# Optimization experiments

Measured on AMD Instinct MI355X. Metric: run time of the kernel, lower is better.

## Reference

```python
import jax, jax.numpy as jnp
import numpy as np


def setup_inputs() -> dict:
    key = jax.random.key(0)
    k1, k2, k3 = jax.random.split(key, 3)
    N, E, C, OUT = 100000, 1000000, 64, 64
    x = jax.random.normal(k1, (N, C), dtype=jnp.float32)
    edge_index = jax.random.randint(k2, (2, E), 0, N, dtype=jnp.int32)
    W = jax.random.normal(k3, (2 * C, OUT), dtype=jnp.float32) * (1.0 / np.sqrt(2 * C))
    b = jnp.zeros((OUT,), dtype=jnp.float32)
    return {"x": x, "edge_index": edge_index, "W": W, "b": b}


def reference(x, edge_index, W, b):
    # MRConv: x_j = scatter_max(x[src] - x[dst], dst); out = relu(cat([x, x_j]) @ W + b)
    N = x.shape[0]
    src, dst = edge_index[0], edge_index[1]
    diff = x[src] - x[dst]                                  # [E, C] gather + diff
    x_j = jax.ops.segment_max(diff, dst, num_segments=N)    # [N, C] scatter-max
    # nodes with no incoming edges get -inf from segment_max; tg fills them with 0
    x_j = jnp.where(jnp.isfinite(x_j), x_j, 0.0)
    h = jnp.concatenate([x, x_j], axis=1)                   # [N, 2C]
    return jax.nn.relu(h @ W + b)                           # [N, OUT]
```

## Files before the change

kernel.cpp:

```cpp
#include <hip/hip_runtime.h>
#include <math.h>

#define SENT 0x007FFFFFu
#define NEGINF_BITS 0xFF800000u
#define NA 256
#define SB_SHIFT 5
#define SB_MASK ((1u << SB_SHIFT) - 1u)
#define NB 32
#define PITCH 68
#define MAXSB 4096
#define CGRID 1024
#define PADROW 32u

typedef __attribute__((ext_vector_type(8))) short bf16x8;
typedef __attribute__((ext_vector_type(4))) float f32x4;

__device__ __forceinline__ unsigned int fmap(float f) {
    unsigned int u = __float_as_uint(f);
    return (u & 0x80000000u) ? ~u : (u | 0x80000000u);
}
__device__ __forceinline__ unsigned int fmap_bits(unsigned int u) {
    return (u & 0x80000000u) ? ~u : (u | 0x80000000u);
}
__device__ __forceinline__ float funmap(unsigned int u) {
    unsigned int bits = (u & 0x80000000u) ? (u ^ 0x80000000u) : ~u;
    return __uint_as_float(bits);
}
__device__ __forceinline__ unsigned short tobf(float f) {
    unsigned int u = __float_as_uint(f);
    u += 0x7FFFu + ((u >> 16) & 1u);
    return (unsigned short)(u >> 16);
}
__device__ __forceinline__ float frombf(unsigned short s) {
    return __uint_as_float((unsigned int)s << 16);
}

__global__ void __launch_bounds__(256) casthist_kernel(const float* __restrict__ x,
                                                       unsigned short* __restrict__ xb,
                                                       long long n,
                                                       const int* __restrict__ ei,
                                                       unsigned* __restrict__ counts2,
                                                       int E, int nsb, int chunk, int cgrid) {
    __shared__ unsigned h[MAXSB];
    if ((int)blockIdx.x < cgrid) {
        long long i = ((long long)blockIdx.x * 256 + threadIdx.x) * 8;
        long long stride = (long long)cgrid * 256 * 8;
        for (; i < n; i += stride) {
            float4 a = *(const float4*)(x + i);
            float4 c = *(const float4*)(x + i + 4);
            uint4 o;
            o.x = (unsigned)tobf(a.x) | ((unsigned)tobf(a.y) << 16);
            o.y = (unsigned)tobf(a.z) | ((unsigned)tobf(a.w) << 16);
            o.z = (unsigned)tobf(c.x) | ((unsigned)tobf(c.y) << 16);
            o.w = (unsigned)tobf(c.z) | ((unsigned)tobf(c.w) << 16);
            *(uint4*)(xb + i) = o;
        }
    } else {
        int hb = (int)blockIdx.x - cgrid;
        for (int t = threadIdx.x; t < nsb; t += 256) h[t] = 0u;
        __syncthreads();
        int beg = hb * chunk;
        int end = min(beg + chunk, E);
        for (int i = beg + threadIdx.x; i < end; i += 256)
            atomicAdd(&h[((unsigned)ei[E + i]) >> SB_SHIFT], 1u);
        __syncthreads();
        for (int t = threadIdx.x; t < nsb; t += 256)
            counts2[(size_t)t * NA + hb] = h[t];
    }
}

__global__ void __launch_bounds__(256) histA_kernel(const int* __restrict__ ei,
                                                    unsigned* __restrict__ counts2,
                                                    int E, int nsb, int chunk) {
    __shared__ unsigned h[MAXSB];
    for (int t = threadIdx.x; t < nsb; t += 256) h[t] = 0u;
    __syncthreads();
    int beg = blockIdx.x * chunk;
    int end = min(beg + chunk, E);
    for (int i = beg + threadIdx.x; i < end; i += 256)
        atomicAdd(&h[((unsigned)ei[E + i]) >> SB_SHIFT], 1u);
    __syncthreads();
    for (int t = threadIdx.x; t < nsb; t += 256)
        counts2[(size_t)t * NA + blockIdx.x] = h[t];
}

__global__ void __launch_bounds__(512) rowscan_kernel(unsigned* __restrict__ counts2,
                                                      unsigned* __restrict__ sbtot, int nsb) {
    int lane = threadIdx.x & 63;
    int sb = blockIdx.x * 8 + (threadIdx.x >> 6);
    if (sb >= nsb) return;
    unsigned* row = counts2 + (size_t)sb * NA;
    uint4 v = *(const uint4*)(row + 4 * lane);
    unsigned local = v.x + v.y + v.z + v.w;
    unsigned incl = local;
    #pragma unroll
    for (int d = 1; d < 64; d <<= 1) {
        unsigned t = __shfl_up(incl, d);
        if (lane >= d) incl += t;
    }
    unsigned e0 = incl - local;
    uint4 o;
    o.x = e0;
    o.y = e0 + v.x;
    o.z = o.y + v.y;
    o.w = o.z + v.z;
    *(uint4*)(row + 4 * lane) = o;
    if (lane == 63) sbtot[sb] = incl;
}

__global__ void __launch_bounds__(1024) sbscan_kernel(const unsigned* __restrict__ sbtot,
                                                      unsigned* __restrict__ sbbase, int nsb) {
    __shared__ unsigned s[1024];
    __shared__ unsigned carry_s;
    if (threadIdx.x == 0) carry_s = 0u;
    __syncthreads();
    for (int chunk = 0; chunk < nsb; chunk += 1024) {
        int i = chunk + threadIdx.x;
        unsigned v = (i < nsb) ? ((sbtot[i] + 15u) & ~15u) : 0u;
        s[threadIdx.x] = v;
        __syncthreads();
        for (int d = 1; d < 1024; d <<= 1) {
            unsigned t = (threadIdx.x >= d) ? s[threadIdx.x - d] : 0u;
            __syncthreads();
            s[threadIdx.x] += t;
            __syncthreads();
        }
        unsigned carry = carry_s;
        if (i < nsb) sbbase[i] = carry + s[threadIdx.x] - v;
        __syncthreads();
        if (threadIdx.x == 1023) carry_s = carry + s[1023];
        __syncthreads();
    }
    if (threadIdx.x == 0) sbbase[nsb] = carry_s;
}

__global__ void __launch_bounds__(256) placeB_kernel(const int* __restrict__ ei,
                                                     const unsigned* __restrict__ counts2,
                                                     const unsigned* __restrict__ sbbase,
                                                     unsigned* __restrict__ ssrc,
                                                     int E, int nsb, int chunk) {
    __shared__ unsigned fill[MAXSB];
    for (int t = threadIdx.x; t < nsb; t += 256)
        fill[t] = sbbase[t] + counts2[(size_t)t * NA + blockIdx.x];
    __syncthreads();
    int beg = blockIdx.x * chunk;
    int end = min(beg + chunk, E);
    for (int i = beg + threadIdx.x; i < end; i += 256) {
        unsigned src = (unsigned)ei[i];
        unsigned dst = (unsigned)ei[E + i];
        unsigned pos = atomicAdd(&fill[dst >> SB_SHIFT], 1u);
        ssrc[pos] = (src << 6) | (dst & SB_MASK);
    }
}

__global__ void __launch_bounds__(256) pad_kernel(const unsigned* __restrict__ sbbase,
                                                  const unsigned* __restrict__ sbtot,
                                                  unsigned* __restrict__ ssrc, int nsb) {
    int i = blockIdx.x * blockDim.x + threadIdx.x;
    if (i >= nsb) return;
    unsigned s = sbbase[i] + sbtot[i];
    unsigned e = sbbase[i + 1];
    for (unsigned j = s; j < e; ++j) ssrc[j] = PADROW;
}

__global__ void __launch_bounds__(256) reduceBf_kernel(const unsigned short* __restrict__ xb,
                                                       const unsigned* __restrict__ sbbase,
                                                       const unsigned* __restrict__ ssrc,
                                                       unsigned short* __restrict__ xj, int N) {
    __shared__ unsigned M[(NB + 1) * PITCH];
    int tid = threadIdx.x;
    int lane = tid & 63;
    int wid = tid >> 6;

    for (int i = tid; i < (NB + 1) * PITCH; i += 256) M[i] = SENT;

    int nodeBase = blockIdx.x * NB;
    int beg = (int)sbbase[blockIdx.x];
    int end = (int)sbbase[blockIdx.x + 1];
    __syncthreads();

    for (int i0 = beg + wid * 16; i0 < end; i0 += 64) {
        int si = __builtin_amdgcn_readfirstlane(i0);
        uint4 q0 = *(const uint4*)(ssrc + si);
        uint4 q1 = *(const uint4*)(ssrc + si + 4);
        uint4 q2 = *(const uint4*)(ssrc + si + 8);
        uint4 q3 = *(const uint4*)(ssrc + si + 12);
        unsigned pp[16] = {q0.x, q0.y, q0.z, q0.w, q1.x, q1.y, q1.z, q1.w,
                           q2.x, q2.y, q2.z, q2.w, q3.x, q3.y, q3.z, q3.w};
        unsigned short vv[16];
        #pragma unroll
        for (int k = 0; k < 16; ++k)
            vv[k] = xb[(pp[k] & 0xFFFFFFC0u) | (unsigned)lane];
        #pragma unroll
        for (int k = 0; k < 16; ++k) {
            unsigned u32 = ((unsigned)vv[k]) << 16;
            atomicMax(&M[(pp[k] & 63u) * PITCH + lane], fmap_bits(u32));
        }
    }
    __syncthreads();

    for (int row = wid; row < NB; row += 4) {
        int n = nodeBase + row;
        if (n < N) {
            unsigned um = M[row * PITCH + lane];
            unsigned short o = 0;
            if (um != SENT) {
                float mx = funmap(um);
                float xv = frombf(xb[(size_t)n * 64 + lane]);
                o = tobf(mx - xv);
            }
            xj[(size_t)n * 64 + lane] = o;
        }
    }
}

__global__ void __launch_bounds__(256) mlpBf_kernel(const unsigned short* __restrict__ xb,
                                                    const unsigned short* __restrict__ xj,
                                                    const float* __restrict__ W,
                                                    const float* __restrict__ b,
                                                    float* __restrict__ out, int N) {
    int lane = threadIdx.x & 63;
    int wid  = threadIdx.x >> 6;
    int r = lane & 15;
    int g = lane >> 4;

    bf16x8 Bf[4][4];
    #pragma unroll
    for (int nt = 0; nt < 4; ++nt)
        #pragma unroll
        for (int kt = 0; kt < 4; ++kt) {
            const float* wp = W + (size_t)(kt * 32 + g * 8) * 64 + nt * 16 + r;
            bf16x8 f;
            #pragma unroll
            for (int j = 0; j < 8; ++j) f[j] = (short)tobf(wp[(size_t)j * 64]);
            Bf[nt][kt] = f;
        }
    float bias[4];
    #pragma unroll
    for (int nt = 0; nt < 4; ++nt) bias[nt] = b[nt * 16 + r];

    int nTiles = (N + 15) >> 4;
    int totalWaves = gridDim.x * 4;
    for (int tile = blockIdx.x * 4 + wid; tile < nTiles; tile += totalWaves) {
        int nodeBase = tile << 4;
        int rowIdx = min(nodeBase + r, N - 1);
        const unsigned short* xp = xb + (size_t)rowIdx * 64;
        const unsigned short* jp = xj + (size_t)rowIdx * 64;

        bf16x8 Af[4];
        #pragma unroll
        for (int kt = 0; kt < 2; ++kt) {
            Af[kt]     = *(const bf16x8*)(xp + kt * 32 + g * 8);
            Af[2 + kt] = *(const bf16x8*)(jp + kt * 32 + g * 8);
        }

        f32x4 acc[4];
        #pragma unroll
        for (int nt = 0; nt < 4; ++nt) {
            f32x4 a = {bias[nt], bias[nt], bias[nt], bias[nt]};
            acc[nt] = a;
        }
        #pragma unroll
        for (int nt = 0; nt < 4; ++nt)
            #pragma unroll
            for (int kt = 0; kt < 4; ++kt)
                acc[nt] = __builtin_amdgcn_mfma_f32_16x16x32_bf16(Af[kt], Bf[nt][kt], acc[nt], 0, 0, 0);

        #pragma unroll
        for (int nt = 0; nt < 4; ++nt)
            #pragma unroll
            for (int reg = 0; reg < 4; ++reg) {
                int nrow = nodeBase + g * 4 + reg;
                if (nrow < N)
                    out[(size_t)nrow * 64 + nt * 16 + r] = fmaxf(acc[nt][reg], 0.0f);
            }
    }
}


__global__ void __launch_bounds__(256) reduceB_kernel(const float* __restrict__ x,
                                                      const unsigned* __restrict__ sbbase,
                                                      const unsigned* __restrict__ ssrc,
                                                      float* __restrict__ xj, int N) {
    __shared__ unsigned M[(NB + 1) * PITCH];
    int tid = threadIdx.x;
    int lane = tid & 63;
    int wid = tid >> 6;

    for (int i = tid; i < (NB + 1) * PITCH; i += 256) M[i] = SENT;

    int nodeBase = blockIdx.x * NB;
    int beg = (int)sbbase[blockIdx.x];
    int end = (int)sbbase[blockIdx.x + 1];
    __syncthreads();

    for (int i0 = beg + wid * 16; i0 < end; i0 += 64) {
        int si = __builtin_amdgcn_readfirstlane(i0);
        uint4 q0 = *(const uint4*)(ssrc + si);
        uint4 q1 = *(const uint4*)(ssrc + si + 4);
        uint4 q2 = *(const uint4*)(ssrc + si + 8);
        uint4 q3 = *(const uint4*)(ssrc + si + 12);
        unsigned pp[16] = {q0.x, q0.y, q0.z, q0.w, q1.x, q1.y, q1.z, q1.w,
                           q2.x, q2.y, q2.z, q2.w, q3.x, q3.y, q3.z, q3.w};
        float vv[16];
        #pragma unroll
        for (int k = 0; k < 16; ++k)
            vv[k] = x[(pp[k] & 0xFFFFFFC0u) | (unsigned)lane];
        #pragma unroll
        for (int k = 0; k < 16; ++k)
            atomicMax(&M[(pp[k] & 63u) * PITCH + lane], fmap(vv[k]));
    }
    __syncthreads();

    for (int row = wid; row < NB; row += 4) {
        int n = nodeBase + row;
        if (n < N) xj[(size_t)n * 64 + lane] = funmap(M[row * PITCH + lane]);
    }
}

template <bool MAPPED>
__global__ void __launch_bounds__(256) mlp_kernel(const float* __restrict__ x,
                                                  const unsigned int* xj,
                                                  const float* __restrict__ W,
                                                  const float* __restrict__ b,
                                                  float* out, int N) {
    int lane = threadIdx.x & 63;
    int wid  = threadIdx.x >> 6;
    int r = lane & 15;
    int g = lane >> 4;

    bf16x8 Bf[4][4];
    #pragma unroll
    for (int nt = 0; nt < 4; ++nt)
        #pragma unroll
        for (int kt = 0; kt < 4; ++kt) {
            const float* wp = W + (size_t)(kt * 32 + g * 8) * 64 + nt * 16 + r;
            bf16x8 f;
            #pragma unroll
            for (int j = 0; j < 8; ++j) f[j] = (short)tobf(wp[(size_t)j * 64]);
            Bf[nt][kt] = f;
        }
    float bias[4];
    #pragma unroll
    for (int nt = 0; nt < 4; ++nt) bias[nt] = b[nt * 16 + r];

    int nTiles = (N + 15) >> 4;
    int totalWaves = gridDim.x * 4;
    for (int tile = blockIdx.x * 4 + wid; tile < nTiles; tile += totalWaves) {
        int nodeBase = tile << 4;
        int rowIdx = min(nodeBase + r, N - 1);
        const float* xp = x + (size_t)rowIdx * 64;
        const unsigned int* jp = xj + (size_t)rowIdx * 64;

        bf16x8 Af[4];
        float xs[2][8];
        #pragma unroll
        for (int kt = 0; kt < 2; ++kt) {
            float4 flo = *(const float4*)(xp + kt * 32 + g * 8);
            float4 fhi = *(const float4*)(xp + kt * 32 + g * 8 + 4);
            xs[kt][0] = flo.x; xs[kt][1] = flo.y; xs[kt][2] = flo.z; xs[kt][3] = flo.w;
            xs[kt][4] = fhi.x; xs[kt][5] = fhi.y; xs[kt][6] = fhi.z; xs[kt][7] = fhi.w;
            bf16x8 f;
            #pragma unroll
            for (int j = 0; j < 8; ++j) f[j] = (short)tobf(xs[kt][j]);
            Af[kt] = f;
        }
        #pragma unroll
        for (int kt = 0; kt < 2; ++kt) {
            uint4 ulo = *(const uint4*)(jp + kt * 32 + g * 8);
            uint4 uhi = *(const uint4*)(jp + kt * 32 + g * 8 + 4);
            unsigned int uu[8] = {ulo.x, ulo.y, ulo.z, ulo.w, uhi.x, uhi.y, uhi.z, uhi.w};
            bf16x8 f;
            #pragma unroll
            for (int j = 0; j < 8; ++j) {
                bool empty;
                float v;
                if (MAPPED) { empty = (uu[j] == SENT); v = funmap(uu[j]); }
                else        { empty = (uu[j] == NEGINF_BITS); v = __uint_as_float(uu[j]); }
                f[j] = (short)tobf(empty ? 0.0f : (v - xs[kt][j]));
            }
            Af[2 + kt] = f;
        }

        f32x4 acc[4];
        #pragma unroll
        for (int nt = 0; nt < 4; ++nt) {
            f32x4 a = {bias[nt], bias[nt], bias[nt], bias[nt]};
            acc[nt] = a;
        }
        #pragma unroll
        for (int nt = 0; nt < 4; ++nt)
            #pragma unroll
            for (int kt = 0; kt < 4; ++kt)
                acc[nt] = __builtin_amdgcn_mfma_f32_16x16x32_bf16(Af[kt], Bf[nt][kt], acc[nt], 0, 0, 0);

        #pragma unroll
        for (int nt = 0; nt < 4; ++nt)
            #pragma unroll
            for (int reg = 0; reg < 4; ++reg) {
                int nrow = nodeBase + g * 4 + reg;
                if (nrow < N)
                    out[(size_t)nrow * 64 + nt * 16 + r] = fmaxf(acc[nt][reg], 0.0f);
            }
    }
}


__global__ void init_kernel(uint4* __restrict__ ws, int n4) {
    int i = blockIdx.x * blockDim.x + threadIdx.x;
    int stride = gridDim.x * blockDim.x;
    uint4 v = make_uint4(SENT, SENT, SENT, SENT);
    for (; i < n4; i += stride) ws[i] = v;
}

__global__ void scatter_kernel(const float* __restrict__ x,
                               const int* __restrict__ ei,
                               unsigned int* __restrict__ ws, int E) {
    long long gid = (long long)blockIdx.x * blockDim.x + threadIdx.x;
    int e = (int)(gid >> 6);
    int lane = (int)(gid & 63);
    if (e >= E) return;
    int src = ei[e];
    int dst = ei[E + e];
    unsigned int m = fmap(x[(size_t)src * 64 + lane]);
    unsigned int* p = ws + (size_t)dst * 64 + lane;
    if (m > *p) atomicMax(p, m);
}

extern "C" void kernel_launch(void* const* d_in, const int* in_sizes, int n_in,
                              void* d_out, int out_size, void* d_ws, size_t ws_size,
                              hipStream_t stream) {
    const float* x  = (const float*)d_in[0];
    const int*   ei = (const int*)d_in[1];
    const float* W  = (const float*)d_in[2];
    const float* b  = (const float*)d_in[3];
    float* out = (float*)d_out;

    int N = in_sizes[0] / 64;
    int E = in_sizes[1] / 2;

    int nsb = (N + NB - 1) >> SB_SHIFT;
    int chunk = (E + NA - 1) / NA;

    size_t counts2_b = (size_t)nsb * NA * 4;
    size_t sbtot_b   = (size_t)((nsb + 63) & ~63) * 4;
    size_t sbbase_b  = (size_t)(nsb + 1 + 63) / 64 * 64 * 4;
    size_t ssrc_b    = ((size_t)E + 16u * (size_t)nsb) * 4;
    size_t xb_b      = (size_t)N * 64 * 2;
    size_t xjb_b     = (size_t)N * 64 * 2;
    size_t xj32_b    = (size_t)N * 64 * 4;
    size_t needB     = counts2_b + sbtot_b + sbbase_b + ssrc_b;
    size_t needA     = needB + xb_b + xjb_b;

    int mgrid = (((N + 15) >> 4) + 3) / 4;

    if (ws_size >= needA && nsb <= MAXSB) {
        char* p = (char*)d_ws;
        unsigned* counts2 = (unsigned*)p; p += counts2_b;
        unsigned* sbtot   = (unsigned*)p; p += sbtot_b;
        unsigned* sbbase  = (unsigned*)p; p += sbbase_b;
        unsigned* ssrc    = (unsigned*)p; p += ssrc_b;
        unsigned short* xb  = (unsigned short*)p; p += xb_b;
        unsigned short* xjb = (unsigned short*)p;

        long long n = (long long)N * 64;
        casthist_kernel<<<CGRID + NA, 256, 0, stream>>>(x, xb, n, ei, counts2, E, nsb, chunk, CGRID);
        rowscan_kernel<<<(nsb + 7) / 8, 512, 0, stream>>>(counts2, sbtot, nsb);
        sbscan_kernel<<<1, 1024, 0, stream>>>(sbtot, sbbase, nsb);
        placeB_kernel<<<NA, 256, 0, stream>>>(ei, counts2, sbbase, ssrc, E, nsb, chunk);
        pad_kernel<<<(nsb + 255) / 256, 256, 0, stream>>>(sbbase, sbtot, ssrc, nsb);
        reduceBf_kernel<<<nsb, 256, 0, stream>>>(xb, sbbase, ssrc, xjb, N);
        mlpBf_kernel<<<mgrid, 256, 0, stream>>>(xb, xjb, W, b, out, N);
    } else if (ws_size >= needB && nsb <= MAXSB) {
        char* p = (char*)d_ws;
        unsigned* counts2 = (unsigned*)p; p += counts2_b;
        unsigned* sbtot   = (unsigned*)p; p += sbtot_b;
        unsigned* sbbase  = (unsigned*)p; p += sbbase_b;
        unsigned* ssrc    = (unsigned*)p; p += ssrc_b;
        float* xjp = (ws_size >= needB + xj32_b) ? (float*)p : (float*)d_out;

        histA_kernel<<<NA, 256, 0, stream>>>(ei, counts2, E, nsb, chunk);
        rowscan_kernel<<<(nsb + 7) / 8, 512, 0, stream>>>(counts2, sbtot, nsb);
        sbscan_kernel<<<1, 1024, 0, stream>>>(sbtot, sbbase, nsb);
        placeB_kernel<<<NA, 256, 0, stream>>>(ei, counts2, sbbase, ssrc, E, nsb, chunk);
        pad_kernel<<<(nsb + 255) / 256, 256, 0, stream>>>(sbbase, sbtot, ssrc, nsb);
        reduceB_kernel<<<nsb, 256, 0, stream>>>(x, sbbase, ssrc, xjp, N);
        mlp_kernel<false><<<mgrid, 256, 0, stream>>>(x, (const unsigned*)xjp, W, b, out, N);
    } else {
        size_t need2 = (size_t)N * 64 * 4;
        unsigned int* scratch = (ws_size >= need2) ? (unsigned int*)d_ws : (unsigned int*)d_out;
        init_kernel<<<2048, 256, 0, stream>>>((uint4*)scratch, N * 16);
        long long sthreads = (long long)E * 64;
        int sblocks = (int)((sthreads + 255) / 256);
        scatter_kernel<<<sblocks, 256, 0, stream>>>(x, ei, scratch, E);
        mlp_kernel<true><<<mgrid, 256, 0, stream>>>(x, scratch, W, b, out, N);
    }
}
```

Baseline: 103.8 us.

## Fuse superblock scan into rowscan via last-block pattern and merge padding into placement

Removes the single-block sbscan kernel by having the last block to finish rowscan, detected through an atomic counter, compute the superblock exclusive scan. The pad kernel is folded into placeB as extra blocks, and the cast/hist, hist and place kernels move to 512-thread blocks. This cuts two kernel launches and the serial gaps between them, at the cost of a global atomic counter that must be reset by the earlier kernel and a last-block scan sized for up to 4096 entries. The folded pad blocks run alongside placement; that is safe because they only write tail slots that placement never touches.

```diff
diff --git a/kernel.cpp b/kernel.cpp
--- a/kernel.cpp
+++ b/kernel.cpp
@@ -9,7 +9,7 @@
 #define NB 32
 #define PITCH 68
 #define MAXSB 4096
-#define CGRID 1024
+#define CG 768
 #define PADROW 32u
 
 typedef __attribute__((ext_vector_type(8))) short bf16x8;
@@ -35,16 +35,17 @@
     return __uint_as_float((unsigned int)s << 16);
 }
 
-__global__ void __launch_bounds__(256) casthist_kernel(const float* __restrict__ x,
+__global__ void __launch_bounds__(512) casthist_kernel(const float* __restrict__ x,
                                                        unsigned short* __restrict__ xb,
                                                        long long n,
                                                        const int* __restrict__ ei,
                                                        unsigned* __restrict__ counts2,
-                                                       int E, int nsb, int chunk, int cgrid) {
+                                                       unsigned* __restrict__ ctrl,
+                                                       int E, int nsb, int chunk) {
     __shared__ unsigned h[MAXSB];
-    if ((int)blockIdx.x < cgrid) {
-        long long i = ((long long)blockIdx.x * 256 + threadIdx.x) * 8;
-        long long stride = (long long)cgrid * 256 * 8;
+    if ((int)blockIdx.x < CG) {
+        long long i = ((long long)blockIdx.x * 512 + threadIdx.x) * 8;
+        long long stride = (long long)CG * 512 * 8;
         for (; i < n; i += stride) {
             float4 a = *(const float4*)(x + i);
             float4 c = *(const float4*)(x + i + 4);
@@ -56,111 +57,142 @@
             *(uint4*)(xb + i) = o;
         }
     } else {
-        int hb = (int)blockIdx.x - cgrid;
-        for (int t = threadIdx.x; t < nsb; t += 256) h[t] = 0u;
+        int hb = (int)blockIdx.x - CG;
+        if (hb == 0 && threadIdx.x == 0) *ctrl = 0u;
+        for (int t = threadIdx.x; t < nsb; t += 512) h[t] = 0u;
         __syncthreads();
         int beg = hb * chunk;
         int end = min(beg + chunk, E);
-        for (int i = beg + threadIdx.x; i < end; i += 256)
+        for (int i = beg + threadIdx.x; i < end; i += 512)
             atomicAdd(&h[((unsigned)ei[E + i]) >> SB_SHIFT], 1u);
         __syncthreads();
-        for (int t = threadIdx.x; t < nsb; t += 256)
+        for (int t = threadIdx.x; t < nsb; t += 512)
             counts2[(size_t)t * NA + hb] = h[t];
     }
 }
 
-__global__ void __launch_bounds__(256) histA_kernel(const int* __restrict__ ei,
+__global__ void __launch_bounds__(512) histA_kernel(const int* __restrict__ ei,
                                                     unsigned* __restrict__ counts2,
+                                                    unsigned* __restrict__ ctrl,
                                                     int E, int nsb, int chunk) {
     __shared__ unsigned h[MAXSB];
-    for (int t = threadIdx.x; t < nsb; t += 256) h[t] = 0u;
+    if (blockIdx.x == 0 && threadIdx.x == 0) *ctrl = 0u;
+    for (int t = threadIdx.x; t < nsb; t += 512) h[t] = 0u;
     __syncthreads();
     int beg = blockIdx.x * chunk;
     int end = min(beg + chunk, E);
-    for (int i = beg + threadIdx.x; i < end; i += 256)
+    for (int i = beg + threadIdx.x; i < end; i += 512)
         atomicAdd(&h[((unsigned)ei[E + i]) >> SB_SHIFT], 1u);
     __syncthreads();
-    for (int t = threadIdx.x; t < nsb; t += 256)
+    for (int t = threadIdx.x; t < nsb; t += 512)
         counts2[(size_t)t * NA + blockIdx.x] = h[t];
 }
 
 __global__ void __launch_bounds__(512) rowscan_kernel(unsigned* __restrict__ counts2,
-                                                      unsigned* __restrict__ sbtot, int nsb) {
-    int lane = threadIdx.x & 63;
-    int sb = blockIdx.x * 8 + (threadIdx.x >> 6);
-    if (sb >= nsb) return;
-    unsigned* row = counts2 + (size_t)sb * NA;
-    uint4 v = *(const uint4*)(row + 4 * lane);
-    unsigned local = v.x + v.y + v.z + v.w;
-    unsigned incl = local;
+                                                      unsigned* __restrict__ sbtot,
+                                                      unsigned* __restrict__ sbbase,
+                                                      unsigned* __restrict__ ctrl, int nsb) {
+    __shared__ unsigned wsum[8];
+    __shared__ int lastFlag;
+    int tid = threadIdx.x;
+    int lane = tid & 63;
+    int wid = tid >> 6;
+    int sb = blockIdx.x * 8 + wid;
+    if (sb < nsb) {
+        unsigned* row = counts2 + (size_t)sb * NA;
+        uint4 v = *(const uint4*)(row + 4 * lane);
+        unsigned local = v.x + v.y + v.z + v.w;
+        unsigned incl = local;
+        #pragma unroll
+        for (int d = 1; d < 64; d <<= 1) {
+            unsigned t = __shfl_up(incl, d);
+            if (lane >= d) incl += t;
+        }
+        unsigned e0 = incl - local;
+        uint4 o;
+        o.x = e0;
+        o.y = e0 + v.x;
+        o.z = o.y + v.y;
+        o.w = o.z + v.z;
+        *(uint4*)(row + 4 * lane) = o;
+        if (lane == 63)
+            __hip_atomic_store(&sbtot[sb], incl, __ATOMIC_RELAXED, __HIP_MEMORY_SCOPE_AGENT);
+    }
+    __syncthreads();
+    if (tid == 0) {
+        unsigned old = __hip_atomic_fetch_add(ctrl, 1u, __ATOMIC_ACQ_REL, __HIP_MEMORY_SCOPE_AGENT);
+        lastFlag = (old == gridDim.x - 1);
+    }
+    __syncthreads();
+    if (!lastFlag) return;
+
+    unsigned excl[8];
+    unsigned run = 0;
+    #pragma unroll
+    for (int i = 0; i < 8; ++i) {
+        int idx = tid * 8 + i;
+        unsigned c = (idx < nsb)
+            ? __hip_atomic_load(&sbtot[idx], __ATOMIC_RELAXED, __HIP_MEMORY_SCOPE_AGENT) : 0u;
+        c = (c + 15u) & ~15u;
+        excl[i] = run;
+        run += c;
+    }
+    unsigned T = run;
+    unsigned incl = T;
     #pragma unroll
     for (int d = 1; d < 64; d <<= 1) {
         unsigned t = __shfl_up(incl, d);
         if (lane >= d) incl += t;
     }
-    unsigned e0 = incl - local;
-    uint4 o;
-    o.x = e0;
-    o.y = e0 + v.x;
-    o.z = o.y + v.y;
-    o.w = o.z + v.z;
-    *(uint4*)(row + 4 * lane) = o;
-    if (lane == 63) sbtot[sb] = incl;
-}
-
-__global__ void __launch_bounds__(1024) sbscan_kernel(const unsigned* __restrict__ sbtot,
-                                                      unsigned* __restrict__ sbbase, int nsb) {
-    __shared__ unsigned s[1024];
-    __shared__ unsigned carry_s;
-    if (threadIdx.x == 0) carry_s = 0u;
-    __syncthreads();
-    for (int chunk = 0; chunk < nsb; chunk += 1024) {
-        int i = chunk + threadIdx.x;
-        unsigned v = (i < nsb) ? ((sbtot[i] + 15u) & ~15u) : 0u;
-        s[threadIdx.x] = v;
-        __syncthreads();
-        for (int d = 1; d < 1024; d <<= 1) {
-            unsigned t = (threadIdx.x >= d) ? s[threadIdx.x - d] : 0u;
-            __syncthreads();
-            s[threadIdx.x] += t;
-            __syncthreads();
-        }
-        unsigned carry = carry_s;
-        if (i < nsb) sbbase[i] = carry + s[threadIdx.x] - v;
-        __syncthreads();
-        if (threadIdx.x == 1023) carry_s = carry + s[1023];
-        __syncthreads();
-    }
-    if (threadIdx.x == 0) sbbase[nsb] = carry_s;
-}
-
-__global__ void __launch_bounds__(256) placeB_kernel(const int* __restrict__ ei,
+    if (lane == 63) wsum[wid] = incl;
+    unsigned texcl = incl - T;
+    __syncthreads();
+    if (wid == 0) {
+        unsigned wv = (lane < 8) ? wsum[lane] : 0u;
+        unsigned wincl = wv;
+        #pragma unroll
+        for (int d = 1; d < 8; d <<= 1) {
+            unsigned t = __shfl_up(wincl, d);
+            if (lane >= d) wincl += t;
+        }
+        if (lane < 8) wsum[lane] = wincl - wv;
+    }
+    __syncthreads();
+    unsigned base = wsum[wid] + texcl;
+    #pragma unroll
+    for (int i = 0; i < 8; ++i) {
+        int idx = tid * 8 + i;
+        if (idx <= nsb) sbbase[idx] = base + excl[i];
+    }
+}
+
+__global__ void __launch_bounds__(512) placeB_kernel(const int* __restrict__ ei,
                                                      const unsigned* __restrict__ counts2,
                                                      const unsigned* __restrict__ sbbase,
+                                                     const unsigned* __restrict__ sbtot,
                                                      unsigned* __restrict__ ssrc,
                                                      int E, int nsb, int chunk) {
+    if ((int)blockIdx.x >= NA) {
+        int i = ((int)blockIdx.x - NA) * 512 + threadIdx.x;
+        if (i < nsb) {
+            unsigned s = sbbase[i] + sbtot[i];
+            unsigned e = sbbase[i + 1];
+            for (unsigned j = s; j < e; ++j) ssrc[j] = PADROW;
+        }
+        return;
+    }
     __shared__ unsigned fill[MAXSB];
-    for (int t = threadIdx.x; t < nsb; t += 256)
+    for (int t = threadIdx.x; t < nsb; t += 512)
         fill[t] = sbbase[t] + counts2[(size_t)t * NA + blockIdx.x];
     __syncthreads();
     int beg = blockIdx.x * chunk;
     int end = min(beg + chunk, E);
-    for (int i = beg + threadIdx.x; i < end; i += 256) {
+    for (int i = beg + threadIdx.x; i < end; i += 512) {
         unsigned src = (unsigned)ei[i];
         unsigned dst = (unsigned)ei[E + i];
         unsigned pos = atomicAdd(&fill[dst >> SB_SHIFT], 1u);
         ssrc[pos] = (src << 6) | (dst & SB_MASK);
     }
-}
-
-__global__ void __launch_bounds__(256) pad_kernel(const unsigned* __restrict__ sbbase,
-                                                  const unsigned* __restrict__ sbtot,
-                                                  unsigned* __restrict__ ssrc, int nsb) {
-    int i = blockIdx.x * blockDim.x + threadIdx.x;
-    if (i >= nsb) return;
-    unsigned s = sbbase[i] + sbtot[i];
-    unsigned e = sbbase[i + 1];
-    for (unsigned j = s; j < e; ++j) ssrc[j] = PADROW;
 }
 
 __global__ void __launch_bounds__(256) reduceBf_kernel(const unsigned short* __restrict__ xb,
@@ -441,34 +473,36 @@
 
     int nsb = (N + NB - 1) >> SB_SHIFT;
     int chunk = (E + NA - 1) / NA;
+    int padB = (nsb + 511) / 512;
 
     size_t counts2_b = (size_t)nsb * NA * 4;
     size_t sbtot_b   = (size_t)((nsb + 63) & ~63) * 4;
     size_t sbbase_b  = (size_t)(nsb + 1 + 63) / 64 * 64 * 4;
+    size_t ctrl_b    = 64;
     size_t ssrc_b    = ((size_t)E + 16u * (size_t)nsb) * 4;
     size_t xb_b      = (size_t)N * 64 * 2;
     size_t xjb_b     = (size_t)N * 64 * 2;
     size_t xj32_b    = (size_t)N * 64 * 4;
-    size_t needB     = counts2_b + sbtot_b + sbbase_b + ssrc_b;
+    size_t needB     = counts2_b + sbtot_b + sbbase_b + ctrl_b + ssrc_b;
     size_t needA     = needB + xb_b + xjb_b;
 
     int mgrid = (((N + 15) >> 4) + 3) / 4;
+    int rsgrid = (nsb + 7) / 8;
 
     if (ws_size >= needA && nsb <= MAXSB) {
         char* p = (char*)d_ws;
         unsigned* counts2 = (unsigned*)p; p += counts2_b;
         unsigned* sbtot   = (unsigned*)p; p += sbtot_b;
         unsigned* sbbase  = (unsigned*)p; p += sbbase_b;
+        unsigned* ctrl    = (unsigned*)p; p += ctrl_b;
         unsigned* ssrc    = (unsigned*)p; p += ssrc_b;
         unsigned short* xb  = (unsigned short*)p; p += xb_b;
         unsigned short* xjb = (unsigned short*)p;
 
         long long n = (long long)N * 64;
-        casthist_kernel<<<CGRID + NA, 256, 0, stream>>>(x, xb, n, ei, counts2, E, nsb, chunk, CGRID);
-        rowscan_kernel<<<(nsb + 7) / 8, 512, 0, stream>>>(counts2, sbtot, nsb);
-        sbscan_kernel<<<1, 1024, 0, stream>>>(sbtot, sbbase, nsb);
-        placeB_kernel<<<NA, 256, 0, stream>>>(ei, counts2, sbbase, ssrc, E, nsb, chunk);
-        pad_kernel<<<(nsb + 255) / 256, 256, 0, stream>>>(sbbase, sbtot, ssrc, nsb);
+        casthist_kernel<<<CG + NA, 512, 0, stream>>>(x, xb, n, ei, counts2, ctrl, E, nsb, chunk);
+        rowscan_kernel<<<rsgrid, 512, 0, stream>>>(counts2, sbtot, sbbase, ctrl, nsb);
+        placeB_kernel<<<NA + padB, 512, 0, stream>>>(ei, counts2, sbbase, sbtot, ssrc, E, nsb, chunk);
         reduceBf_kernel<<<nsb, 256, 0, stream>>>(xb, sbbase, ssrc, xjb, N);
         mlpBf_kernel<<<mgrid, 256, 0, stream>>>(xb, xjb, W, b, out, N);
     } else if (ws_size >= needB && nsb <= MAXSB) {
@@ -476,14 +510,13 @@
         unsigned* counts2 = (unsigned*)p; p += counts2_b;
         unsigned* sbtot   = (unsigned*)p; p += sbtot_b;
         unsigned* sbbase  = (unsigned*)p; p += sbbase_b;
+        unsigned* ctrl    = (unsigned*)p; p += ctrl_b;
         unsigned* ssrc    = (unsigned*)p; p += ssrc_b;
         float* xjp = (ws_size >= needB + xj32_b) ? (float*)p : (float*)d_out;
 
-        histA_kernel<<<NA, 256, 0, stream>>>(ei, counts2, E, nsb, chunk);
-        rowscan_kernel<<<(nsb + 7) / 8, 512, 0, stream>>>(counts2, sbtot, nsb);
-        sbscan_kernel<<<1, 1024, 0, stream>>>(sbtot, sbbase, nsb);
-        placeB_kernel<<<NA, 256, 0, stream>>>(ei, counts2, sbbase, ssrc, E, nsb, chunk);
-        pad_kernel<<<(nsb + 255) / 256, 256, 0, stream>>>(sbbase, sbtot, ssrc, nsb);
+        histA_kernel<<<NA, 512, 0, stream>>>(ei, counts2, ctrl, E, nsb, chunk);
+        rowscan_kernel<<<rsgrid, 512, 0, stream>>>(counts2, sbtot, sbbase, ctrl, nsb);
+        placeB_kernel<<<NA + padB, 512, 0, stream>>>(ei, counts2, sbbase, sbtot, ssrc, E, nsb, chunk);
         reduceB_kernel<<<nsb, 256, 0, stream>>>(x, sbbase, ssrc, xjp, N);
         mlp_kernel<false><<<mgrid, 256, 0, stream>>>(x, (const unsigned*)xjp, W, b, out, N);
     } else {
```

Result: faster. 94.70 us (-8.8%).
